# Performance work log

Measured on AMD Instinct MI355X. Metric: run time of the kernel, lower is better.

Reference implementation:

```python
import jax, jax.numpy as jnp
import numpy as np

QUERY_DIM = 1024
HIDDEN_DIM = 1024


def setup_inputs() -> dict:
    key = jax.random.key(0)
    k1, k2, k3, k4 = jax.random.split(key, 4)
    query = jax.random.normal(k1, (8, 2048, QUERY_DIM), dtype=jnp.float32)
    info = jax.random.normal(k2, (8, 2048, HIDDEN_DIM), dtype=jnp.float32)
    # nn.Linear params: weight [out, in], bias [out]
    bound = 1.0 / np.sqrt(QUERY_DIM)
    W = jax.random.uniform(k3, (HIDDEN_DIM, QUERY_DIM), jnp.float32, -bound, bound)
    b = jax.random.uniform(k4, (HIDDEN_DIM,), jnp.float32, -bound, bound)
    return {"query": query, "info": info, "W": W, "b": b}


def reference(query, info, W, b):
    # Eval mode: dropout is identity.
    # projected query: [B, S, hidden]
    q = jnp.einsum("bsq,hq->bsh", query, W) + b
    # unscaled attention scores over info rows: [B, S, M]
    scores = jax.nn.softmax(jnp.einsum("bsh,bmh->bsm", q, info), axis=-1)
    # weighted sum of info: [B, S, hidden]
    return jnp.einsum("bsm,bmh->bsh", scores, info)
```

## Files before the change

### kernel.cpp

```cpp
#include <hip/hip_runtime.h>

#define DEVI __device__ __forceinline__

typedef __attribute__((ext_vector_type(4))) float f32x4;
typedef __attribute__((ext_vector_type(8))) short bf16x8;

typedef const unsigned __attribute__((address_space(1))) as1_u32;
typedef unsigned __attribute__((address_space(3))) as3_u32;

DEVI unsigned fbits(float x){ union{float f;unsigned u;} v; v.f=x; return v.u; }
DEVI float bitsf(unsigned u){ union{unsigned u;float f;} v; v.u=u; return v.f; }
DEVI short bf_rne(float x){ unsigned u=fbits(x); u += 0x7fffu + ((u>>16)&1u); return (short)(u>>16); }

DEVI unsigned pack_hi2(unsigned u0, unsigned u1){
#if __has_builtin(__builtin_amdgcn_perm)
  return __builtin_amdgcn_perm(u1, u0, 0x07060302u);
#else
  return (u0 >> 16) | (u1 & 0xffff0000u);
#endif
}
DEVI unsigned pack_rne2(float a, float b){
  return (unsigned)(unsigned short)bf_rne(a) | ((unsigned)(unsigned short)bf_rne(b) << 16);
}

DEVI void gload16(const short* g, short* s){
  __builtin_amdgcn_global_load_lds((as1_u32*)g, (as3_u32*)s, 16, 0, 0);
}

#define SBAR() { __builtin_amdgcn_sched_barrier(0); asm volatile("" ::: "memory"); \
                 __builtin_amdgcn_s_barrier(); __builtin_amdgcn_sched_barrier(0); }

#define MF(a,b,c) __builtin_amdgcn_mfma_f32_16x16x32_bf16(a,b,c,0,0,0)
#define MROW(M, x) \
  acc[M][0] = MF(x, bb0, acc[M][0]); \
  acc[M][1] = MF(x, bb1, acc[M][1]); \
  acc[M][2] = MF(x, bb2, acc[M][2]); \
  acc[M][3] = MF(x, bb3, acc[M][3]);

__global__ __launch_bounds__(256)
void k_split(const float* __restrict__ in, short* __restrict__ hi,
             short* __restrict__ lo, const long n4)
{
  long i = (long)blockIdx.x*256 + threadIdx.x;
  const long stride = (long)gridDim.x*256;
  for (; i < n4; i += stride){
    const float4 v = ((const float4*)in)[i];
    const unsigned u0=fbits(v.x), u1=fbits(v.y), u2=fbits(v.z), u3=fbits(v.w);
    ((uint2*)hi)[i] = make_uint2(pack_hi2(u0,u1), pack_hi2(u2,u3));
    const float l0 = v.x - bitsf(u0 & 0xffff0000u);
    const float l1 = v.y - bitsf(u1 & 0xffff0000u);
    const float l2 = v.z - bitsf(u2 & 0xffff0000u);
    const float l3 = v.w - bitsf(u3 & 0xffff0000u);
    ((uint2*)lo)[i] = make_uint2(pack_rne2(l0,l1), pack_rne2(l2,l3));
  }
}

template<bool BIAS, bool SPLIT_OUT>
__global__ __launch_bounds__(512, 2)
void k_gemm3(const short* __restrict__ Ah, const short* __restrict__ Al,
             const short* __restrict__ Bh, const short* __restrict__ Bl,
             void* __restrict__ Cv, const float* __restrict__ bias,
             const int K, const int lda, const int ldb, const int ldc,
             const long sAz, const long sBz, const long sCz, const int loOff)
{
  __shared__ short LDS[65536];

  const int tid = threadIdx.x;
  const int w = tid >> 6, l = tid & 63;
  const int wr = w >> 2, wc = w & 3;
  const int fr = l & 15, h4 = l >> 4;
  const long bz = blockIdx.z;

  const int nwg = gridDim.x * gridDim.y;
  const int xy  = blockIdx.y * gridDim.x + blockIdx.x;
  const int q8  = nwg >> 3;
  const int sw  = (xy & 7) * q8 + (xy >> 3);
  const int bx  = sw % gridDim.x;
  const int by  = sw / gridDim.x;

  const size_t aOff = (size_t)bz*sAz + (size_t)bx*256*lda;
  const size_t bOff = (size_t)bz*sBz + (size_t)by*256*ldb;

  const int c0 = w*64 + l, c1 = c0 + 512;
  const int k0 = ((c0 & 3) ^ ((c0 >> 3) & 3)) * 8;
  const int k1 = ((c1 & 3) ^ ((c1 >> 3) & 3)) * 8;
  const size_t a0 = (size_t)(c0 >> 2)*lda + k0;
  const size_t a1 = (size_t)(c1 >> 2)*lda + k1;
  const size_t b0 = (size_t)(c0 >> 2)*ldb + k0;
  const size_t b1 = (size_t)(c1 >> 2)*ldb + k1;
  const int dS0 = w*512, dS1 = 4096 + w*512;

  const int cswz = (h4 ^ ((fr >> 1) & 3)) << 3;
  const int rbA = (wr*128 + fr)*32 + cswz;
  const int rbB = 16384 + (wc*64 + fr)*32 + cswz;

  f32x4 acc[8][4];
#pragma unroll
  for (int m = 0; m < 8; ++m)
#pragma unroll
    for (int n = 0; n < 4; ++n){ acc[m][n][0]=0.f; acc[m][n][1]=0.f; acc[m][n][2]=0.f; acc[m][n][3]=0.f; }

  const short* pAh = Ah + aOff;
  const short* pAl = Al + aOff;
  const short* pBh = Bh + bOff;
  const short* pBl = Bl + bOff;

  gload16(pAh + a0, LDS + dS0);
  gload16(pAh + a1, LDS + dS1);
  gload16(pBh + b0, LDS + 16384 + dS0);
  gload16(pBh + b1, LDS + 16384 + dS1);
  gload16(pAl + a0, LDS + 8192 + dS0);
  gload16(pAl + a1, LDS + 8192 + dS1);
  gload16(pBl + b0, LDS + 24576 + dS0);
  gload16(pBl + b1, LDS + 24576 + dS1);
  pAh += 32; pAl += 32; pBh += 32; pBl += 32;

#define STEP3(CO, PF, V1, V2, V3)                                            \
{                                                                            \
  const short* pA = LDS + (CO) + rbA;                                        \
  const short* pB = LDS + (CO) + rbB;                                        \
  short* dst = LDS + ((CO) ^ 32768);                                         \
  bf16x8 ah0,ah1,ah2,ah3,ah4,ah5,ah6,ah7, bb0,bb1,bb2,bb3;                   \
                                                            \
  asm volatile("s_waitcnt vmcnt(" V1 ")" ::: "memory");                      \
  SBAR();                                                                    \
  if (PF){ gload16(pAh + a0, dst + dS0);                                     \
           gload16(pAh + a1, dst + dS1);                                     \
           gload16(pBh + b0, dst + 16384 + dS0);                             \
           gload16(pBh + b1, dst + 16384 + dS1); }                           \
  bb0 = *(const bf16x8*)(pB);                                                \
  bb1 = *(const bf16x8*)(pB + 512);                                          \
  bb2 = *(const bf16x8*)(pB + 1024);                                         \
  bb3 = *(const bf16x8*)(pB + 1536);                                         \
  ah0 = *(const bf16x8*)(pA);                                                \
  ah1 = *(const bf16x8*)(pA + 512);                                          \
  ah2 = *(const bf16x8*)(pA + 1024);                                         \
  ah3 = *(const bf16x8*)(pA + 1536);                                         \
  ah4 = *(const bf16x8*)(pA + 2048);                                         \
  ah5 = *(const bf16x8*)(pA + 2560);                                         \
  ah6 = *(const bf16x8*)(pA + 3072);                                         \
  ah7 = *(const bf16x8*)(pA + 3584);                                         \
  __builtin_amdgcn_s_setprio(1);                                             \
  MROW(0,ah0) MROW(1,ah1) MROW(2,ah2) MROW(3,ah3)                            \
  MROW(4,ah4) MROW(5,ah5) MROW(6,ah6) MROW(7,ah7)                            \
  __builtin_amdgcn_s_setprio(0);                                             \
                                                            \
  asm volatile("s_waitcnt vmcnt(" V2 ")" ::: "memory");                      \
  SBAR();                                                                    \
  if (PF){ gload16(pAl + a0, dst + 8192 + dS0);                              \
           gload16(pAl + a1, dst + 8192 + dS1);                              \
           gload16(pBl + b0, dst + 24576 + dS0);                             \
           gload16(pBl + b1, dst + 24576 + dS1);                             \
           pAh += 32; pAl += 32; pBh += 32; pBl += 32; }                     \
  {                                                                          \
    bf16x8 al0 = *(const bf16x8*)(pA + 8192);                                \
    bf16x8 al1 = *(const bf16x8*)(pA + 8192 + 512);                          \
    bf16x8 al2 = *(const bf16x8*)(pA + 8192 + 1024);                         \
    bf16x8 al3 = *(const bf16x8*)(pA + 8192 + 1536);                         \
    bf16x8 al4 = *(const bf16x8*)(pA + 8192 + 2048);                         \
    bf16x8 al5 = *(const bf16x8*)(pA + 8192 + 2560);                         \
    bf16x8 al6 = *(const bf16x8*)(pA + 8192 + 3072);                         \
    bf16x8 al7 = *(const bf16x8*)(pA + 8192 + 3584);                         \
    __builtin_amdgcn_s_setprio(1);                                           \
    MROW(0,al0) MROW(1,al1) MROW(2,al2) MROW(3,al3)                          \
    MROW(4,al4) MROW(5,al5) MROW(6,al6) MROW(7,al7)                          \
    __builtin_amdgcn_s_setprio(0);                                           \
  }                                                                          \
                                   \
  asm volatile("s_waitcnt vmcnt(" V3 ")" ::: "memory");                      \
  SBAR();                                                                    \
  bb0 = *(const bf16x8*)(pB + 8192);                                         \
  bb1 = *(const bf16x8*)(pB + 8192 + 512);                                   \
  bb2 = *(const bf16x8*)(pB + 8192 + 1024);                                  \
  bb3 = *(const bf16x8*)(pB + 8192 + 1536);                                  \
  __builtin_amdgcn_s_setprio(1);                                             \
  MROW(0,ah0) MROW(1,ah1) MROW(2,ah2) MROW(3,ah3)                            \
  MROW(4,ah4) MROW(5,ah5) MROW(6,ah6) MROW(7,ah7)                            \
  __builtin_amdgcn_s_setprio(0);                                             \
}

  const int nk = K >> 5;
#pragma unroll 1
  for (int it = 0; it < nk - 2; it += 2){
    STEP3(0,     1, "4", "6", "8")
    STEP3(32768, 1, "4", "6", "8")
  }
  STEP3(0,     1, "4", "6", "8")
  STEP3(32768, 0, "4", "2", "0")

#undef STEP3

  const int rr = h4*4;
  if constexpr (SPLIT_OUT){
    short* Ch = (short*)Cv + (size_t)bz*sCz
              + (size_t)(bx*256 + wr*128)*ldc + by*256 + wc*64;
    short* Cl = Ch + loOff;
#pragma unroll
    for (int n = 0; n < 4; ++n){
      const int col = n*16 + fr;
      const float bv = BIAS ? bias[by*256 + wc*64 + col] : 0.f;
#pragma unroll
      for (int m = 0; m < 8; ++m)
#pragma unroll
        for (int j = 0; j < 4; ++j){
          const float v = acc[m][n][j] + bv;
          const unsigned uh = fbits(v) & 0xffff0000u;
          const size_t idx = (size_t)(m*16 + rr + j)*ldc + col;
          Ch[idx] = (short)(uh >> 16);
          Cl[idx] = bf_rne(v - bitsf(uh));
        }
    }
  } else {
    float* C = (float*)Cv + (size_t)bz*sCz
             + (size_t)(bx*256 + wr*128)*ldc + by*256 + wc*64;
#pragma unroll
    for (int n = 0; n < 4; ++n){
      const int col = n*16 + fr;
      const float bv = BIAS ? bias[by*256 + wc*64 + col] : 0.f;
#pragma unroll
      for (int m = 0; m < 8; ++m)
#pragma unroll
        for (int j = 0; j < 4; ++j)
          C[(size_t)(m*16 + rr + j)*ldc + col] = acc[m][n][j] + bv;
    }
  }
}

__global__ __launch_bounds__(512, 2)
void k_gemm1(const short* __restrict__ Ah, const short* __restrict__ Bh,
             void* __restrict__ Cv,
             const int K, const int lda, const int ldb, const int ldc,
             const long sAz, const long sBz, const long sCz)
{
  __shared__ short LDS[65536];

  const int tid = threadIdx.x;
  const int w = tid >> 6, l = tid & 63;
  const int wr = w >> 2, wc = w & 3;
  const int fr = l & 15, h4 = l >> 4;
  const long bz = blockIdx.z;

  const int nwg = gridDim.x * gridDim.y;
  const int xy  = blockIdx.y * gridDim.x + blockIdx.x;
  const int q8  = nwg >> 3;
  const int sw  = (xy & 7) * q8 + (xy >> 3);
  const int bx  = sw % gridDim.x;
  const int by  = sw / gridDim.x;

  const size_t aOff = (size_t)bz*sAz + (size_t)bx*256*lda;
  const size_t bOff = (size_t)bz*sBz + (size_t)by*256*ldb;

  const int sch = (((l & 7) ^ ((l >> 3) & 7)) << 3);
  const int rA0 = wr*128 + (w & 3)*8 + (l >> 3);
  int aoffg[4];
#pragma unroll
  for (int q2 = 0; q2 < 4; ++q2) aoffg[q2] = (rA0 + 32*q2)*lda;
  const int rB0 = wc*64 + (w >> 2)*8 + (l >> 3);
  int boffg[4];
#pragma unroll
  for (int j2 = 0; j2 < 4; ++j2) boffg[j2] = (rB0 + 16*j2)*ldb;
  const int dAu = wr*8192 + (w & 3)*512;
  const int dBu = 16384 + wc*4096 + (w >> 2)*512;

  const int rbA = (wr*128 + fr)*64;
  const int rbB = 16384 + (wc*64 + fr)*64;
  const int c08 = ((h4     ) ^ (l & 7)) << 3;
  const int c18 = ((h4 + 4 ) ^ (l & 7)) << 3;

  f32x4 acc[8][4];
#pragma unroll
  for (int m = 0; m < 8; ++m)
#pragma unroll
    for (int n = 0; n < 4; ++n){ acc[m][n][0]=0.f; acc[m][n][1]=0.f; acc[m][n][2]=0.f; acc[m][n][3]=0.f; }

  const short* Asrc = Ah + aOff + sch;
  const short* Bsrc = Bh + bOff + sch;

  {
    short* dB0 = LDS + dBu;
    short* dA0 = LDS + dAu;
    gload16(Bsrc + boffg[0], dB0);
    gload16(Bsrc + boffg[1], dB0 + 1024);
    gload16(Bsrc + boffg[2], dB0 + 2048);
    gload16(Bsrc + boffg[3], dB0 + 3072);
    gload16(Asrc + aoffg[0], dA0);
    gload16(Asrc + aoffg[1], dA0 + 2048);
    gload16(Asrc + aoffg[2], dA0 + 4096);
    gload16(Asrc + aoffg[3], dA0 + 6144);
  }
  Asrc += 64; Bsrc += 64;
  asm volatile("s_waitcnt vmcnt(2)" ::: "memory");
  SBAR();

#define TILE(CO, PF, VA, VB)                                                 \
{                                                                            \
  const short* pA = LDS + (CO) + rbA;                                        \
  const short* pB = LDS + (CO) + rbB;                                        \
  short* dAp = LDS + ((CO)^32768) + dAu;                                     \
  short* dBp = LDS + ((CO)^32768) + dBu;                                     \
  bf16x8 aA,aB,aC,aD, bb0,bb1,bb2,bb3;                                       \
  if (PF){ gload16(Bsrc + boffg[0], dBp); gload16(Bsrc + boffg[1], dBp + 1024); } \
  bb0 = *(const bf16x8*)(pB +        c08);                                   \
  bb1 = *(const bf16x8*)(pB + 1024 + c08);                                   \
  bb2 = *(const bf16x8*)(pB + 2048 + c08);                                   \
  bb3 = *(const bf16x8*)(pB + 3072 + c08);                                   \
  aA  = *(const bf16x8*)(pA +        c08);                                   \
  aB  = *(const bf16x8*)(pA + 1024 + c08);                                   \
  aC  = *(const bf16x8*)(pA + 2048 + c08);                                   \
  aD  = *(const bf16x8*)(pA + 3072 + c08);                                   \
  SBAR();                                                                    \
  __builtin_amdgcn_s_setprio(1);                                             \
  MROW(0,aA) MROW(1,aB) MROW(2,aC) MROW(3,aD)                                \
  __builtin_amdgcn_s_setprio(0);                                             \
  asm volatile("s_waitcnt vmcnt(" VA ")" ::: "memory");                      \
  SBAR();                                                                    \
  if (PF){ gload16(Bsrc + boffg[2], dBp + 2048); gload16(Bsrc + boffg[3], dBp + 3072); } \
  aA = *(const bf16x8*)(pA + 4096 + c08);                                    \
  aB = *(const bf16x8*)(pA + 5120 + c08);                                    \
  aC = *(const bf16x8*)(pA + 6144 + c08);                                    \
  aD = *(const bf16x8*)(pA + 7168 + c08);                                    \
  SBAR();                                                                    \
  __builtin_amdgcn_s_setprio(1);                                             \
  MROW(4,aA) MROW(5,aB) MROW(6,aC) MROW(7,aD)                                \
  __builtin_amdgcn_s_setprio(0);                                             \
  SBAR();                                                                    \
  if (PF){ gload16(Asrc + aoffg[0], dAp); gload16(Asrc + aoffg[1], dAp + 2048); } \
  bb0 = *(const bf16x8*)(pB +        c18);                                   \
  bb1 = *(const bf16x8*)(pB + 1024 + c18);                                   \
  bb2 = *(const bf16x8*)(pB + 2048 + c18);                                   \
  bb3 = *(const bf16x8*)(pB + 3072 + c18);                                   \
  aA  = *(const bf16x8*)(pA +        c18);                                   \
  aB  = *(const bf16x8*)(pA + 1024 + c18);                                   \
  aC  = *(const bf16x8*)(pA + 2048 + c18);                                   \
  aD  = *(const bf16x8*)(pA + 3072 + c18);                                   \
  SBAR();                                                                    \
  __builtin_amdgcn_s_setprio(1);                                             \
  MROW(0,aA) MROW(1,aB) MROW(2,aC) MROW(3,aD)                                \
  __builtin_amdgcn_s_setprio(0);                                             \
  SBAR();                                                                    \
  if (PF){ gload16(Asrc + aoffg[2], dAp + 4096); gload16(Asrc + aoffg[3], dAp + 6144); } \
  aA = *(const bf16x8*)(pA + 4096 + c18);                                    \
  aB = *(const bf16x8*)(pA + 5120 + c18);                                    \
  aC = *(const bf16x8*)(pA + 6144 + c18);                                    \
  aD = *(const bf16x8*)(pA + 7168 + c18);                                    \
  SBAR();                                                                    \
  __builtin_amdgcn_s_setprio(1);                                             \
  MROW(4,aA) MROW(5,aB) MROW(6,aC) MROW(7,aD)                                \
  __builtin_amdgcn_s_setprio(0);                                             \
  if (PF){ Asrc += 64; Bsrc += 64; }                                         \
  asm volatile("s_waitcnt vmcnt(" VB ")" ::: "memory");                      \
  SBAR();                                                                    \
}

  const int nkt = K >> 6;
#pragma unroll 1
  for (int it = 0; it < nkt - 2; it += 2){
    TILE(0,     1, "2", "2")
    TILE(32768, 1, "2", "2")
  }
  TILE(0,     1, "2", "2")
  TILE(32768, 0, "0", "0")

#undef TILE

  const int rr = h4*4;
  float* C = (float*)Cv + (size_t)bz*sCz
           + (size_t)(bx*256 + wr*128)*ldc + by*256 + wc*64;
#pragma unroll
  for (int n = 0; n < 4; ++n){
    const int col = n*16 + fr;
#pragma unroll
    for (int m = 0; m < 8; ++m)
#pragma unroll
      for (int j = 0; j < 4; ++j)
        C[(size_t)(m*16 + rr + j)*ldc + col] = acc[m][n][j];
  }
}

__global__ __launch_bounds__(256)
void k_prep_info(const float* __restrict__ V, short* __restrict__ hi,
                 short* __restrict__ lo, short* __restrict__ T,
                 const int MM, const int DD, const long sVz, const long sTz)
{
  __shared__ float t[64][65];
  const float* Vb = V + (long)blockIdx.z*sVz;
  short* hb = hi + (long)blockIdx.z*sVz;
  short* lb = lo + (long)blockIdx.z*sVz;
  short* Tb = T  + (long)blockIdx.z*sTz;
  const int m0 = blockIdx.x*64, d0 = blockIdx.y*64;
  const int tid = threadIdx.x;
#pragma unroll
  for (int i = 0; i < 4; ++i){
    const int c = tid + 256*i;
    const int r = c >> 4, c4 = (c & 15)*4;
    const float4 v = *(const float4*)(Vb + (size_t)(m0 + r)*DD + d0 + c4);
    t[r][c4+0]=v.x; t[r][c4+1]=v.y; t[r][c4+2]=v.z; t[r][c4+3]=v.w;
    const unsigned u0=fbits(v.x), u1=fbits(v.y), u2=fbits(v.z), u3=fbits(v.w);
    const size_t gi = (size_t)(m0 + r)*DD + d0 + c4;
    *(uint2*)(hb + gi) = make_uint2(pack_hi2(u0,u1), pack_hi2(u2,u3));
    const float l0 = v.x - bitsf(u0 & 0xffff0000u);
    const float l1 = v.y - bitsf(u1 & 0xffff0000u);
    const float l2 = v.z - bitsf(u2 & 0xffff0000u);
    const float l3 = v.w - bitsf(u3 & 0xffff0000u);
    *(uint2*)(lb + gi) = make_uint2(pack_rne2(l0,l1), pack_rne2(l2,l3));
  }
  __syncthreads();
#pragma unroll
  for (int i = 0; i < 4; ++i){
    const int c = tid + 256*i;
    const int d = c >> 4, m4 = (c & 15)*4;
    short4 o;
    o.x = bf_rne(t[m4+0][d]); o.y = bf_rne(t[m4+1][d]);
    o.z = bf_rne(t[m4+2][d]); o.w = bf_rne(t[m4+3][d]);
    *(short4*)(Tb + (size_t)(d0 + d)*MM + m0 + m4) = o;
  }
}

__global__ __launch_bounds__(256)
void k_softmax_rows(float* __restrict__ Sb, const long sz)
{
  float* row = Sb + (long)blockIdx.y*sz + (long)blockIdx.x*2048;
  short* prow = (short*)row;
  const int tid = threadIdx.x;
  const int lane = tid & 63, wid = tid >> 6;

  const float4 v0 = *(const float4*)(row + tid*4);
  const float4 v1 = *(const float4*)(row + 1024 + tid*4);
  float x[8] = {v0.x, v0.y, v0.z, v0.w, v1.x, v1.y, v1.z, v1.w};

  float mx = x[0];
#pragma unroll
  for (int j = 1; j < 8; ++j) mx = fmaxf(mx, x[j]);
#pragma unroll
  for (int off = 32; off; off >>= 1) mx = fmaxf(mx, __shfl_xor(mx, off));

  __shared__ float red[8];
  if (lane == 0) red[wid] = mx;
  __syncthreads();
  mx = fmaxf(fmaxf(red[0], red[1]), fmaxf(red[2], red[3]));

  float e[8]; float s = 0.f;
#pragma unroll
  for (int j = 0; j < 8; ++j){ e[j] = __expf(x[j] - mx); s += e[j]; }
#pragma unroll
  for (int off = 32; off; off >>= 1) s += __shfl_xor(s, off);
  if (lane == 0) red[4 + wid] = s;
  __syncthreads();
  s = (red[4] + red[5]) + (red[6] + red[7]);
  const float inv = 1.0f / s;

  *(uint2*)(prow + tid*4)        = make_uint2(pack_rne2(e[0]*inv, e[1]*inv), pack_rne2(e[2]*inv, e[3]*inv));
  *(uint2*)(prow + 1024 + tid*4) = make_uint2(pack_rne2(e[4]*inv, e[5]*inv), pack_rne2(e[6]*inv, e[7]*inv));
}

extern "C" void kernel_launch(void* const* d_in, const int* in_sizes, int n_in,
                              void* d_out, int out_size, void* d_ws, size_t ws_size,
                              hipStream_t stream)
{
  const float* query = (const float*)d_in[0];
  const float* info  = (const float*)d_in[1];
  const float* Wm    = (const float*)d_in[2];
  const float* bias  = (const float*)d_in[3];
  float* out = (float*)d_out;

  const int B = 8, S = 2048, M = 2048, D = 1024;
  const size_t PB = (size_t)S * D;

  short* info_hi = (short*)d_ws;
  short* info_lo = info_hi + 16777216;
  short* infoT   = info_lo + 16777216;
  short* W_hi    = infoT   + 16777216;
  short* W_lo    = W_hi    + 1048576;
  float* Sbuf    = (float*)(W_lo + 1048576);
  const size_t sb = (size_t)S * M * sizeof(float);
  size_t avail = ws_size > 104857600ull ? ws_size - 104857600ull : 0;
  int nchunk = (int)(avail / sb); if (nchunk > 8) nchunk = 8; if (nchunk < 1) nchunk = 1;

  short* q_s = (short*)d_out;
  const long qBz = 2*(long)PB;
  const int  qLo = (int)PB;

  k_split<<<1024, 256, 0, stream>>>(Wm, W_hi, W_lo, (long)(D*D/4));

  int nb = 2*nchunk; if (nb > 8) nb = 8;
  for (int q0 = 0; q0 < B; q0 += nb){
    const int cur = (q0 + nb <= B) ? nb : (B - q0);
    short* qt_hi = (short*)Sbuf;
    short* qt_lo = qt_hi + (size_t)cur*PB;
    k_split<<<2048, 256, 0, stream>>>(query + (size_t)q0*PB, qt_hi, qt_lo,
                                      (long)((size_t)cur*PB/4));
    k_gemm3<true, true><<<dim3(S/256, D/256, cur), 512, 0, stream>>>(
        qt_hi, qt_lo, W_hi, W_lo, q_s + (size_t)q0*qBz, bias,
        D, D, D, D, (long)PB, 0L, qBz, qLo);
  }

  k_prep_info<<<dim3(M/64, D/64, B), 256, 0, stream>>>(
      info, info_hi, info_lo, infoT, M, D, (long)PB, (long)PB);

  for (int b0 = 0; b0 < B; b0 += nchunk){
    const int cur = (b0 + nchunk <= B) ? nchunk : (B - b0);

    const short* qh = q_s + (size_t)b0*qBz;
    k_gemm3<false, false><<<dim3(S/256, M/256, cur), 512, 0, stream>>>(
        qh, qh + qLo, info_hi + (size_t)b0*PB, info_lo + (size_t)b0*PB,
        Sbuf, nullptr, D, D, D, M, qBz, (long)PB, (long)S*M, 0);

    k_softmax_rows<<<dim3(S, cur), 256, 0, stream>>>(Sbuf, (long)S*M);

    k_gemm1<<<dim3(S/256, D/256, cur), 512, 0, stream>>>(
        (const short*)Sbuf, infoT + (size_t)b0*PB,
        out + (size_t)b0*PB, M, 2*M, M, D,
        (long)(2*(size_t)S*M), (long)PB, (long)S*D);
  }
}
```

Measured before the change: 439.0 us.

## Issue full-tile prefetch up front and use one barrier per K step

Both GEMM main loops now issue all global-to-LDS prefetch loads for the next tile at the start of each step, followed by a sched_barrier. They then run the MFMA phases with no intermediate barriers and finish with a single vmcnt(0) wait and one barrier. This removes several workgroup barriers and partial vmcnt waits per K step, cutting sync overhead. The trade-off is coarser overlap, since every step now waits for all outstanding loads at its end, which could expose memory latency if the compute phase is shorter than the load time.

```diff
diff --git a/kernel.cpp b/kernel.cpp
--- a/kernel.cpp
+++ b/kernel.cpp
@@ -114,20 +114,27 @@
   gload16(pBl + b0, LDS + 24576 + dS0);
   gload16(pBl + b1, LDS + 24576 + dS1);
   pAh += 32; pAl += 32; pBh += 32; pBl += 32;
-
-#define STEP3(CO, PF, V1, V2, V3)                                            \
+  asm volatile("s_waitcnt vmcnt(0)" ::: "memory");
+  SBAR();
+
+#define STEP3(CO, PF)                                                        \
 {                                                                            \
   const short* pA = LDS + (CO) + rbA;                                        \
   const short* pB = LDS + (CO) + rbB;                                        \
   short* dst = LDS + ((CO) ^ 32768);                                         \
   bf16x8 ah0,ah1,ah2,ah3,ah4,ah5,ah6,ah7, bb0,bb1,bb2,bb3;                   \
-                                                            \
-  asm volatile("s_waitcnt vmcnt(" V1 ")" ::: "memory");                      \
-  SBAR();                                                                    \
+   \
   if (PF){ gload16(pAh + a0, dst + dS0);                                     \
            gload16(pAh + a1, dst + dS1);                                     \
            gload16(pBh + b0, dst + 16384 + dS0);                             \
-           gload16(pBh + b1, dst + 16384 + dS1); }                           \
+           gload16(pBh + b1, dst + 16384 + dS1);                             \
+           gload16(pAl + a0, dst + 8192 + dS0);                              \
+           gload16(pAl + a1, dst + 8192 + dS1);                              \
+           gload16(pBl + b0, dst + 24576 + dS0);                             \
+           gload16(pBl + b1, dst + 24576 + dS1);                             \
+           pAh += 32; pAl += 32; pBh += 32; pBl += 32; }                     \
+  __builtin_amdgcn_sched_barrier(0);                                         \
+                                                            \
   bb0 = *(const bf16x8*)(pB);                                                \
   bb1 = *(const bf16x8*)(pB + 512);                                          \
   bb2 = *(const bf16x8*)(pB + 1024);                                         \
@@ -145,13 +152,6 @@
   MROW(4,ah4) MROW(5,ah5) MROW(6,ah6) MROW(7,ah7)                            \
   __builtin_amdgcn_s_setprio(0);                                             \
                                                             \
-  asm volatile("s_waitcnt vmcnt(" V2 ")" ::: "memory");                      \
-  SBAR();                                                                    \
-  if (PF){ gload16(pAl + a0, dst + 8192 + dS0);                              \
-           gload16(pAl + a1, dst + 8192 + dS1);                              \
-           gload16(pBl + b0, dst + 24576 + dS0);                             \
-           gload16(pBl + b1, dst + 24576 + dS1);                             \
-           pAh += 32; pAl += 32; pBh += 32; pBl += 32; }                     \
   {                                                                          \
     bf16x8 al0 = *(const bf16x8*)(pA + 8192);                                \
     bf16x8 al1 = *(const bf16x8*)(pA + 8192 + 512);                          \
@@ -167,8 +167,6 @@
     __builtin_amdgcn_s_setprio(0);                                           \
   }                                                                          \
                                    \
-  asm volatile("s_waitcnt vmcnt(" V3 ")" ::: "memory");                      \
-  SBAR();                                                                    \
   bb0 = *(const bf16x8*)(pB + 8192);                                         \
   bb1 = *(const bf16x8*)(pB + 8192 + 512);                                   \
   bb2 = *(const bf16x8*)(pB + 8192 + 1024);                                  \
@@ -177,16 +175,19 @@
   MROW(0,ah0) MROW(1,ah1) MROW(2,ah2) MROW(3,ah3)                            \
   MROW(4,ah4) MROW(5,ah5) MROW(6,ah6) MROW(7,ah7)                            \
   __builtin_amdgcn_s_setprio(0);                                             \
+                                           \
+  asm volatile("s_waitcnt vmcnt(0)" ::: "memory");                           \
+  SBAR();                                                                    \
 }
 
   const int nk = K >> 5;
 #pragma unroll 1
   for (int it = 0; it < nk - 2; it += 2){
-    STEP3(0,     1, "4", "6", "8")
-    STEP3(32768, 1, "4", "6", "8")
-  }
-  STEP3(0,     1, "4", "6", "8")
-  STEP3(32768, 0, "4", "2", "0")
+    STEP3(0,     1)
+    STEP3(32768, 1)
+  }
+  STEP3(0,     1)
+  STEP3(32768, 0)
 
 #undef STEP3
 
@@ -289,17 +290,27 @@
     gload16(Asrc + aoffg[3], dA0 + 6144);
   }
   Asrc += 64; Bsrc += 64;
-  asm volatile("s_waitcnt vmcnt(2)" ::: "memory");
+  asm volatile("s_waitcnt vmcnt(0)" ::: "memory");
   SBAR();
 
-#define TILE(CO, PF, VA, VB)                                                 \
+#define TILE(CO, PF)                                                         \
 {                                                                            \
   const short* pA = LDS + (CO) + rbA;                                        \
   const short* pB = LDS + (CO) + rbB;                                        \
   short* dAp = LDS + ((CO)^32768) + dAu;                                     \
   short* dBp = LDS + ((CO)^32768) + dBu;                                     \
   bf16x8 aA,aB,aC,aD, bb0,bb1,bb2,bb3;                                       \
-  if (PF){ gload16(Bsrc + boffg[0], dBp); gload16(Bsrc + boffg[1], dBp + 1024); } \
+  if (PF){ gload16(Bsrc + boffg[0], dBp);                                    \
+           gload16(Bsrc + boffg[1], dBp + 1024);                             \
+           gload16(Bsrc + boffg[2], dBp + 2048);                             \
+           gload16(Bsrc + boffg[3], dBp + 3072);                             \
+           gload16(Asrc + aoffg[0], dAp);                                    \
+           gload16(Asrc + aoffg[1], dAp + 2048);                             \
+           gload16(Asrc + aoffg[2], dAp + 4096);                             \
+           gload16(Asrc + aoffg[3], dAp + 6144);                             \
+           Asrc += 64; Bsrc += 64; }                                         \
+  __builtin_amdgcn_sched_barrier(0);                                         \
+                                                                    \
   bb0 = *(const bf16x8*)(pB +        c08);                                   \
   bb1 = *(const bf16x8*)(pB + 1024 + c08);                                   \
   bb2 = *(const bf16x8*)(pB + 2048 + c08);                                   \
@@ -308,23 +319,17 @@
   aB  = *(const bf16x8*)(pA + 1024 + c08);                                   \
   aC  = *(const bf16x8*)(pA + 2048 + c08);                                   \
   aD  = *(const bf16x8*)(pA + 3072 + c08);                                   \
-  SBAR();                                                                    \
   __builtin_amdgcn_s_setprio(1);                                             \
   MROW(0,aA) MROW(1,aB) MROW(2,aC) MROW(3,aD)                                \
   __builtin_amdgcn_s_setprio(0);                                             \
-  asm volatile("s_waitcnt vmcnt(" VA ")" ::: "memory");                      \
-  SBAR();                                                                    \
-  if (PF){ gload16(Bsrc + boffg[2], dBp + 2048); gload16(Bsrc + boffg[3], dBp + 3072); } \
   aA = *(const bf16x8*)(pA + 4096 + c08);                                    \
   aB = *(const bf16x8*)(pA + 5120 + c08);                                    \
   aC = *(const bf16x8*)(pA + 6144 + c08);                                    \
   aD = *(const bf16x8*)(pA + 7168 + c08);                                    \
-  SBAR();                                                                    \
   __builtin_amdgcn_s_setprio(1);                                             \
   MROW(4,aA) MROW(5,aB) MROW(6,aC) MROW(7,aD)                                \
   __builtin_amdgcn_s_setprio(0);                                             \
-  SBAR();                                                                    \
-  if (PF){ gload16(Asrc + aoffg[0], dAp); gload16(Asrc + aoffg[1], dAp + 2048); } \
+                                                                    \
   bb0 = *(const bf16x8*)(pB +        c18);                                   \
   bb1 = *(const bf16x8*)(pB + 1024 + c18);                                   \
   bb2 = *(const bf16x8*)(pB + 2048 + c18);                                   \
@@ -333,33 +338,28 @@
   aB  = *(const bf16x8*)(pA + 1024 + c18);                                   \
   aC  = *(const bf16x8*)(pA + 2048 + c18);                                   \
   aD  = *(const bf16x8*)(pA + 3072 + c18);                                   \
-  SBAR();                                                                    \
   __builtin_amdgcn_s_setprio(1);                                             \
   MROW(0,aA) MROW(1,aB) MROW(2,aC) MROW(3,aD)                                \
   __builtin_amdgcn_s_setprio(0);                                             \
-  SBAR();                                                                    \
-  if (PF){ gload16(Asrc + aoffg[2], dAp + 4096); gload16(Asrc + aoffg[3], dAp + 6144); } \
   aA = *(const bf16x8*)(pA + 4096 + c18);                                    \
   aB = *(const bf16x8*)(pA + 5120 + c18);                                    \
   aC = *(const bf16x8*)(pA + 6144 + c18);                                    \
   aD = *(const bf16x8*)(pA + 7168 + c18);                                    \
-  SBAR();                                                                    \
   __builtin_amdgcn_s_setprio(1);                                             \
   MROW(4,aA) MROW(5,aB) MROW(6,aC) MROW(7,aD)                                \
   __builtin_amdgcn_s_setprio(0);                                             \
-  if (PF){ Asrc += 64; Bsrc += 64; }                                         \
-  asm volatile("s_waitcnt vmcnt(" VB ")" ::: "memory");                      \
+  asm volatile("s_waitcnt vmcnt(0)" ::: "memory");                           \
   SBAR();                                                                    \
 }
 
   const int nkt = K >> 6;
 #pragma unroll 1
   for (int it = 0; it < nkt - 2; it += 2){
-    TILE(0,     1, "2", "2")
-    TILE(32768, 1, "2", "2")
-  }
-  TILE(0,     1, "2", "2")
-  TILE(32768, 0, "0", "0")
+    TILE(0,     1)
+    TILE(32768, 1)
+  }
+  TILE(0,     1)
+  TILE(32768, 0)
 
 #undef TILE
 
```

After: 444.8 us. Within noise of the previous version (+1.3%).
